# Performance work log

Hardware: AMD Instinct MI355X
Metric: run time of the kernel (lower is better)

Reference implementation:

```python
import jax, jax.numpy as jnp
import numpy as np

PSZ = 3      # patch_size
TOPK = 2     # topk candidates
EPS = 1e-12  # F.normalize eps


def extract_patches(x, psz, stride):
    """Torch unfold-style patch extraction: (B,C,H,W) -> (B, nH*nW, C, psz, psz)."""
    B, C, H, W = x.shape
    nH = (H - psz) // stride + 1
    nW = (W - psz) // stride + 1
    slices = []
    for di in range(psz):          # fixed 3x3 loop, not a data-dim loop
        for dj in range(psz):
            slices.append(x[:, :, di:di + (nH - 1) * stride + 1:stride,
                                  dj:dj + (nW - 1) * stride + 1:stride])
    p = jnp.stack(slices, axis=-1)                      # (B,C,nH,nW,psz*psz)
    p = p.reshape(B, C, nH, nW, psz, psz)
    p = p.transpose(0, 2, 3, 1, 4, 5).reshape(B, nH * nW, C, psz, psz)
    return p


def l2_normalize(x, axis):
    n = jnp.sqrt(jnp.sum(x * x, axis=axis, keepdims=True))
    return x / jnp.maximum(n, EPS)


def setup_inputs() -> dict:
    key = jax.random.key(0)
    k1, k2 = jax.random.split(key)
    pred_style = jax.random.normal(k1, (2, 128, 48, 48), dtype=jnp.float32)
    target_style = jax.random.normal(k2, (2 * TOPK, 128, 48, 48), dtype=jnp.float32)
    return {"pred_style": pred_style, "target_style": target_style}


def reference(pred_style, target_style):
    B = pred_style.shape[0]
    # raw patches (used for the final MSE / gather)
    tp = extract_patches(target_style, PSZ, 1)   # (B*TOPK, nT, C, 3, 3)
    pp = extract_patches(pred_style, PSZ, 1)     # (B, nQ, C, 3, 3)
    nT = tp.shape[1]

    # matching is done on channel-normalized features (F.normalize dim=1 / dim=2)
    p1n = extract_patches(l2_normalize(pred_style, axis=1), PSZ, 1)  # (B,nQ,C,3,3)
    tpn = l2_normalize(tp, axis=2).reshape(B, TOPK, nT, *tp.shape[2:])

    # cosine cross-correlation == conv with candidate patches as filters
    scores = jnp.einsum('bqcij,bkncij->bknq', p1n, tpn)  # (B,TOPK,nT,nQ)->(B,TOPK,nQ) reduce below

    sv = jnp.max(scores, axis=2)      # (B, TOPK, nQ) best value per candidate set
    si = jnp.argmax(scores, axis=2)   # (B, TOPK, nQ) best spatial idx per k
    k_idx = jnp.argmax(sv, axis=1)    # (B, nQ) best k per query position
    spatial = jnp.take_along_axis(si, k_idx[:, None, :], axis=1)[:, 0]  # (B, nQ)

    tpr = tp.reshape(B, TOPK, nT, *tp.shape[2:])
    bi = jnp.arange(B)[:, None]
    gathered = tpr[bi, k_idx, spatial]  # (B, nQ, C, 3, 3)

    return jnp.mean((pp - gathered) ** 2)
```

## Files before the change

### kernel.cpp

```cpp
#include <hip/hip_runtime.h>
#include <hip/hip_bf16.h>

typedef unsigned short u16;
typedef __attribute__((ext_vector_type(8))) short short8;
typedef _Float16 half8 __attribute__((ext_vector_type(8)));
typedef __attribute__((ext_vector_type(4))) float f32x4;
typedef __attribute__((ext_vector_type(4))) unsigned int u32x4;

#define CC    128
#define WW    48
#define HW2   2304
#define NHW   46
#define NQ    2116
#define NPIX  2304
#define DSTRIDE ((size_t)NPIX * NPIX + 64)
#define BATCH 2
#define MT    126
#define NTC   190
#define DTS   200

__device__ __forceinline__ u16 f2bf(float f) {
  union { float f; unsigned u; } x; x.f = f;
  unsigned r = (x.u + 0x7fffu + ((x.u >> 16) & 1u)) >> 16;
  return (u16)r;
}

__global__ __launch_bounds__(256) void k_norm(const float* __restrict__ pred,
                                              const float* __restrict__ targ,
                                              u16* __restrict__ PnT, u16* __restrict__ TnT) {
  const int img = blockIdx.y;
  const int p0  = blockIdx.x * 64;
  const int tid = threadIdx.x;
  const float* src = img < 2 ? pred + (size_t)img * CC * HW2
                             : targ + (size_t)(img - 2) * CC * HW2;
  u16* out = img < 2 ? PnT + (size_t)img * NPIX * CC
                     : TnT + (size_t)(img - 2) * NPIX * CC;

  __shared__ float sT[64][129];
  __shared__ float sInv[64];

  #pragma unroll
  for (int it = 0; it < 32; ++it) {
    int idx = it * 256 + tid;
    int c = idx >> 6, p = idx & 63;
    sT[p][c] = src[(size_t)c * HW2 + p0 + p];
  }
  __syncthreads();
  if (tid < 64) {
    float s = 0.f;
    for (int c = 0; c < CC; ++c) { float v = sT[tid][c]; s += v * v; }
    sInv[tid] = 1.0f / fmaxf(sqrtf(s), 1e-12f);
  }
  __syncthreads();
  #pragma unroll
  for (int it = 0; it < 4; ++it) {
    int cid = it * 256 + tid;
    int p = cid >> 4, g = cid & 15;
    int r = p0 + p;
    int sc = (g & ~7) | ((g & 7) ^ (r & 7));
    float inv = sInv[p];
    unsigned pack[4];
    #pragma unroll
    for (int e = 0; e < 8; ++e) {
      float v = sT[p][sc * 8 + e] * inv;
      if ((e & 1) == 0) pack[e >> 1] = (unsigned)f2bf(v);
      else              pack[e >> 1] |= ((unsigned)f2bf(v)) << 16;
    }
    u32x4 o; o.x = pack[0]; o.y = pack[1]; o.z = pack[2]; o.w = pack[3];
    *reinterpret_cast<u32x4*>(out + (size_t)r * CC + g * 8) = o;
  }
}

__global__ __launch_bounds__(512, 2) void k_pixdotH(const u16* __restrict__ PnT, const u16* __restrict__ TnT,
                                                    u16* __restrict__ H) {
  __shared__ u16 buf[40960];
  u16* sA = buf;
  u16* sB = buf + 16384;
  const int nt = blockIdx.x, mt = blockIdx.y, s = blockIdx.z;
  const int tid = threadIdx.x, lane = tid & 63, wid = tid >> 6;
  const int wm = wid >> 2, wn = wid & 3;
  const int r15 = lane & 15, g16 = lane >> 4;
  const int m0 = mt * MT, n0 = nt * NTC;

  const u16* Ab = PnT + (size_t)(s >> 1) * NPIX * CC;
  const u16* Bb = TnT + (size_t)s * NPIX * CC;
  u16* Hs = H + (size_t)s * DSTRIDE;

  #pragma unroll
  for (int i = 0; i < 4; ++i) {
    int sl = i * 512 + tid;
    int row = m0 + (sl >> 4); row = row < 2303 ? row : 2303;
    __builtin_amdgcn_global_load_lds(
      (const __attribute__((address_space(1))) unsigned*)(Ab + (size_t)row * CC + (sl & 15) * 8),
      (__attribute__((address_space(3))) unsigned*)&sA[sl * 8], 16, 0, 0);
  }
  #pragma unroll
  for (int i = 0; i < 6; ++i) {
    int sl = i * 512 + tid;
    int row = n0 + (sl >> 4); row = row < 2303 ? row : 2303;
    __builtin_amdgcn_global_load_lds(
      (const __attribute__((address_space(1))) unsigned*)(Bb + (size_t)row * CC + (sl & 15) * 8),
      (__attribute__((address_space(3))) unsigned*)&sB[sl * 8], 16, 0, 0);
  }

  f32x4 acc[4][3];
  const f32x4 z4 = {0.f, 0.f, 0.f, 0.f};
  #pragma unroll
  for (int i = 0; i < 4; ++i)
    #pragma unroll
    for (int j = 0; j < 3; ++j) acc[i][j] = z4;

  asm volatile("s_waitcnt vmcnt(0)" ::: "memory");
  __builtin_amdgcn_s_barrier();

  const int arow0 = wm * 64 + r15;
  const int brow0 = wn * 48 + r15;
  #pragma unroll
  for (int ks = 0; ks < 4; ++ks) {
    const int c = ks * 4 + g16;
    short8 af[4], bfv[3];
    #pragma unroll
    for (int mi = 0; mi < 4; ++mi) {
      int row = arow0 + mi * 16;
      int gr = m0 + row;
      af[mi] = *reinterpret_cast<const short8*>(
        &sA[row * 128 + (c >> 3) * 64 + (((c & 7) ^ (gr & 7)) * 8)]);
    }
    #pragma unroll
    for (int ni = 0; ni < 3; ++ni) {
      int row = brow0 + ni * 16;
      int gr = n0 + row;
      bfv[ni] = *reinterpret_cast<const short8*>(
        &sB[row * 128 + (c >> 3) * 64 + (((c & 7) ^ (gr & 7)) * 8)]);
    }
    __builtin_amdgcn_s_setprio(1);
    #pragma unroll
    for (int mi = 0; mi < 4; ++mi)
      #pragma unroll
      for (int ni = 0; ni < 3; ++ni)
        acc[mi][ni] = __builtin_amdgcn_mfma_f32_16x16x32_bf16(af[mi], bfv[ni], acc[mi][ni], 0, 0, 0);
    __builtin_amdgcn_s_setprio(0);
  }

  __syncthreads();
  u16* Dt = buf;
  #pragma unroll
  for (int mi = 0; mi < 4; ++mi)
    #pragma unroll
    for (int ni = 0; ni < 3; ++ni) {
      int col = wn * 48 + ni * 16 + r15;
      #pragma unroll
      for (int rg = 0; rg < 4; ++rg) {
        int row = wm * 64 + mi * 16 + g16 * 4 + rg;
        Dt[row * DTS + col] = __builtin_bit_cast(u16, (_Float16)acc[mi][ni][rg]);
      }
    }
  __syncthreads();

  for (int t = tid; t < 126 * 24; t += 512) {
    int rr = t / 24, c8 = t - rr * 24;
    int grow = m0 + rr;
    if (grow >= 2302) continue;
    int lcol = c8 * 8;
    int lim = NTC - lcol;
    int glim = 2302 - (n0 + lcol);
    lim = lim < glim ? lim : glim;
    if (lim <= 0) continue;
    int base = rr * DTS + lcol;
    half8 a0 = *reinterpret_cast<const half8*>(&Dt[base]);
    half8 b0 = *reinterpret_cast<const half8*>(&Dt[base + DTS]);
    half8 b1 = *reinterpret_cast<const half8*>(&Dt[base + DTS + 8]);
    half8 c0 = *reinterpret_cast<const half8*>(&Dt[base + 2 * DTS]);
    half8 c1 = *reinterpret_cast<const half8*>(&Dt[base + 2 * DTS + 8]);
    half8 s1v = __builtin_shufflevector(b0, b1, 1, 2, 3, 4, 5, 6, 7, 8);
    half8 s2v = __builtin_shufflevector(c0, c1, 2, 3, 4, 5, 6, 7, 8, 9);
    half8 sum = a0 + s1v + s2v;
    u32x4 pk = __builtin_bit_cast(u32x4, sum);
    u16* dst = Hs + (size_t)grow * NPIX + n0 + lcol;
    int nd = lim >= 8 ? 4 : (lim >> 1);
    #pragma unroll
    for (int d = 0; d < 4; ++d)
      if (d < nd) *reinterpret_cast<unsigned*>(dst + 2 * d) = pk[d];
  }
}

__global__ __launch_bounds__(512) void k_stencil(const u16* __restrict__ H,
                                                 const float* __restrict__ pred,
                                                 const float* __restrict__ targ,
                                                 float* __restrict__ msep) {
  const int bid = blockIdx.x;
  const int b = bid >= 1058 ? 1 : 0;
  const int j = bid - b * 1058;
  const int xcd = j & 7, pos = j >> 3;
  const int jswz = (xcd < 2 ? xcd * 133 : 266 + (xcd - 2) * 132) + pos;

  const int tid = threadIdx.x;
  const int hid = tid >> 8, htid = tid & 255;
  const int lane = tid & 63, wid = tid >> 6;
  const int q = jswz * 2 + hid;
  const int qy = q / NHW, qx = q - qy * NHW;
  const int qp = qy * WW + qx;

  const _Float16 ninf = __builtin_bit_cast(_Float16, (u16)0xFC00);
  const half8 ninf8 = {ninf, ninf, ninf, ninf, ninf, ninf, ninf, ninf};

  half8 smc[3];
  int nb[3];
  smc[0] = ninf8; smc[1] = ninf8; smc[2] = ninf8;
  nb[0] = nb[1] = nb[2] = 0;

  half8 pmax = ninf8;
  #pragma unroll
  for (int it = 0; it < 3; ++it) {
    int t = it * 256 + htid;
    if (t < 552) {
      int kc = t / 276; int rem = t - kc * 276;
      int ny = rem / 6, cx = rem - ny * 6;
      const u16* Hs = H + (size_t)(b * 2 + kc) * DSTRIDE;
      int colb = ny * 48 + cx * 8;
      half8 t0 = *reinterpret_cast<const half8*>(Hs + (size_t)qp * NPIX + colb);
      half8 t1 = *reinterpret_cast<const half8*>(Hs + (size_t)(qp + 48) * NPIX + colb + 48);
      half8 t2 = *reinterpret_cast<const half8*>(Hs + (size_t)(qp + 96) * NPIX + colb + 96);
      half8 sm = t0 + t1 + t2;
      if (cx == 5) { sm[6] = ninf; sm[7] = ninf; }
      smc[it] = sm;
      nb[it] = kc * NQ + ny * NHW + cx * 8;
      pmax = __builtin_elementwise_max(pmax, sm);
    }
  }
  float m = (float)pmax[0];
  #pragma unroll
  for (int e = 1; e < 8; ++e) { float v = (float)pmax[e]; m = v > m ? v : m; }
  #pragma unroll
  for (int off = 1; off < 64; off <<= 1) {
    float o = __shfl_xor(m, off, 64);
    m = o > m ? o : m;
  }
  __shared__ float sv[8];
  __shared__ int si[8];
  __shared__ float rsum[8];
  if (lane == 0) sv[wid] = m;
  __syncthreads();
  float M = sv[hid * 4];
  #pragma unroll
  for (int wv = 1; wv < 4; ++wv) { float v = sv[hid * 4 + wv]; M = v > M ? v : M; }

  int nmin = 0x7fffffff;
  if (m == M) {
    #pragma unroll
    for (int it = 0; it < 3; ++it) {
      #pragma unroll
      for (int e = 0; e < 8; ++e) {
        float sc = (float)smc[it][e];
        int n = nb[it] + e;
        if (sc == M && n < nmin) nmin = n;
      }
    }
  }
  #pragma unroll
  for (int off = 1; off < 64; off <<= 1) {
    int o = __shfl_xor(nmin, off, 64);
    nmin = o < nmin ? o : nmin;
  }
  if (lane == 0) si[wid] = nmin;
  __syncthreads();
  int fi = si[hid * 4];
  #pragma unroll
  for (int wv = 1; wv < 4; ++wv) { int v = si[hid * 4 + wv]; fi = v < fi ? v : fi; }

  int nkc = fi >= NQ ? 1 : 0;
  int ns = fi - nkc * NQ;
  ns = ns < NQ ? ns : NQ - 1;
  int ny = ns / NHW, nx = ns - ny * NHW;
  const float* P = pred + (size_t)b * CC * HW2;
  const float* T = targ + (size_t)(b * 2 + nkc) * CC * HW2;
  float ssum = 0.f;
  for (int i = htid; i < CC * 9; i += 256) {
    int c = i / 9, sp = i - 9 * c;
    int di = sp / 3, dj = sp - 3 * di;
    float d = P[(size_t)c * HW2 + (qy + di) * WW + qx + dj]
            - T[(size_t)c * HW2 + (ny + di) * WW + nx + dj];
    ssum += d * d;
  }
  #pragma unroll
  for (int off = 1; off < 64; off <<= 1) ssum += __shfl_xor(ssum, off, 64);
  if (lane == 0) rsum[wid] = ssum;
  __syncthreads();
  if (htid == 0) {
    float t = 0.f;
    #pragma unroll
    for (int wv = 0; wv < 4; ++wv) t += rsum[hid * 4 + wv];
    msep[b * NQ + q] = t;
  }
}

__global__ void k_final(const float* __restrict__ msep, float* __restrict__ out) {
  int t = threadIdx.x;
  float s = 0.f;
  for (int i = t; i < BATCH * NQ; i += 256) s += msep[i];
  __shared__ float red[256];
  red[t] = s; __syncthreads();
  for (int st = 128; st > 0; st >>= 1) { if (t < st) red[t] += red[t + st]; __syncthreads(); }
  if (t == 0) out[0] = red[0] * (1.0f / 4875264.0f);
}

extern "C" void kernel_launch(void* const* d_in, const int* in_sizes, int n_in,
                              void* d_out, int out_size, void* d_ws, size_t ws_size,
                              hipStream_t stream) {
  const float* pred = (const float*)d_in[0];
  const float* targ = (const float*)d_in[1];
  char* ws = (char*)d_ws;

  size_t offP = 0;
  size_t offT = offP + (size_t)2 * NPIX * CC * 2;
  size_t offH = offT + (size_t)4 * NPIX * CC * 2;
  size_t offM = offH + (size_t)4 * DSTRIDE * 2;

  u16*   PnT  = (u16*)(ws + offP);
  u16*   TnT  = (u16*)(ws + offT);
  u16*   Hbuf = (u16*)(ws + offH);
  float* msep = (float*)(ws + offM);

  k_norm<<<dim3(36, 6), 256, 0, stream>>>(pred, targ, PnT, TnT);
  k_pixdotH<<<dim3(13, 19, 4), 512, 0, stream>>>(PnT, TnT, Hbuf);
  k_stencil<<<dim3(2 * 1058), 512, 0, stream>>>(Hbuf, pred, targ, msep);
  k_final<<<1, 256, 0, stream>>>(msep, (float*)d_out);
}
```

Measured before the change: 67.39 us.

## Split K-dimension staging into halves to overlap loads with MFMA

The A and B tiles are loaded into LDS as two K-halves (channels 0-63 and 64-127) in separate buffers. The MFMAs on the first half run while the second half's global-to-LDS loads are still in flight, hiding part of the load latency. The epilogue also skips writing H rows whose pixel column is 46 or 47, which are not valid patch positions. This relies on downstream kernels never reading those rows, and it adds one extra barrier.

```diff
diff --git a/kernel.cpp b/kernel.cpp
--- a/kernel.cpp
+++ b/kernel.cpp
@@ -74,8 +74,8 @@
 __global__ __launch_bounds__(512, 2) void k_pixdotH(const u16* __restrict__ PnT, const u16* __restrict__ TnT,
                                                     u16* __restrict__ H) {
   __shared__ u16 buf[40960];
-  u16* sA = buf;
-  u16* sB = buf + 16384;
+  u16* sAh[2] = { buf, buf + 8192 };
+  u16* sBh[2] = { buf + 16384, buf + 28672 };
   const int nt = blockIdx.x, mt = blockIdx.y, s = blockIdx.z;
   const int tid = threadIdx.x, lane = tid & 63, wid = tid >> 6;
   const int wm = wid >> 2, wn = wid & 3;
@@ -86,22 +86,28 @@
   const u16* Bb = TnT + (size_t)s * NPIX * CC;
   u16* Hs = H + (size_t)s * DSTRIDE;
 
-  #pragma unroll
-  for (int i = 0; i < 4; ++i) {
-    int sl = i * 512 + tid;
-    int row = m0 + (sl >> 4); row = row < 2303 ? row : 2303;
-    __builtin_amdgcn_global_load_lds(
-      (const __attribute__((address_space(1))) unsigned*)(Ab + (size_t)row * CC + (sl & 15) * 8),
-      (__attribute__((address_space(3))) unsigned*)&sA[sl * 8], 16, 0, 0);
-  }
-  #pragma unroll
-  for (int i = 0; i < 6; ++i) {
-    int sl = i * 512 + tid;
-    int row = n0 + (sl >> 4); row = row < 2303 ? row : 2303;
-    __builtin_amdgcn_global_load_lds(
-      (const __attribute__((address_space(1))) unsigned*)(Bb + (size_t)row * CC + (sl & 15) * 8),
-      (__attribute__((address_space(3))) unsigned*)&sB[sl * 8], 16, 0, 0);
-  }
+  auto stageA = [&](int h) {
+    #pragma unroll
+    for (int i = 0; i < 2; ++i) {
+      int idx = i * 512 + tid;
+      int row = idx >> 3, lc = idx & 7;
+      int grow = m0 + row; grow = grow < 2303 ? grow : 2303;
+      __builtin_amdgcn_global_load_lds(
+        (const __attribute__((address_space(1))) unsigned*)(Ab + (size_t)grow * CC + (h * 8 + lc) * 8),
+        (__attribute__((address_space(3))) unsigned*)&sAh[h][idx * 8], 16, 0, 0);
+    }
+  };
+  auto stageB = [&](int h) {
+    #pragma unroll
+    for (int i = 0; i < 3; ++i) {
+      int idx = i * 512 + tid;
+      int row = idx >> 3, lc = idx & 7;
+      int grow = n0 + row; grow = grow < 2303 ? grow : 2303;
+      __builtin_amdgcn_global_load_lds(
+        (const __attribute__((address_space(1))) unsigned*)(Bb + (size_t)grow * CC + (h * 8 + lc) * 8),
+        (__attribute__((address_space(3))) unsigned*)&sBh[h][idx * 8], 16, 0, 0);
+    }
+  };
 
   f32x4 acc[4][3];
   const f32x4 z4 = {0.f, 0.f, 0.f, 0.f};
@@ -110,37 +116,47 @@
     #pragma unroll
     for (int j = 0; j < 3; ++j) acc[i][j] = z4;
 
+  const int arow0 = wm * 64 + r15;
+  const int brow0 = wn * 48 + r15;
+
+  auto mfmaPair = [&](int ks0) {
+    #pragma unroll
+    for (int ks = ks0; ks < ks0 + 2; ++ks) {
+      const int c = ks * 4 + g16;
+      const int h = c >> 3, lc = c & 7;
+      short8 af[4], bfv[3];
+      #pragma unroll
+      for (int mi = 0; mi < 4; ++mi) {
+        int row = arow0 + mi * 16;
+        int gr = m0 + row;
+        af[mi] = *reinterpret_cast<const short8*>(
+          &sAh[h][row * 64 + ((lc ^ (gr & 7)) * 8)]);
+      }
+      #pragma unroll
+      for (int ni = 0; ni < 3; ++ni) {
+        int row = brow0 + ni * 16;
+        int gr = n0 + row;
+        bfv[ni] = *reinterpret_cast<const short8*>(
+          &sBh[h][row * 64 + ((lc ^ (gr & 7)) * 8)]);
+      }
+      __builtin_amdgcn_s_setprio(1);
+      #pragma unroll
+      for (int mi = 0; mi < 4; ++mi)
+        #pragma unroll
+        for (int ni = 0; ni < 3; ++ni)
+          acc[mi][ni] = __builtin_amdgcn_mfma_f32_16x16x32_bf16(af[mi], bfv[ni], acc[mi][ni], 0, 0, 0);
+      __builtin_amdgcn_s_setprio(0);
+    }
+  };
+
+  stageA(0); stageB(0);
   asm volatile("s_waitcnt vmcnt(0)" ::: "memory");
   __builtin_amdgcn_s_barrier();
-
-  const int arow0 = wm * 64 + r15;
-  const int brow0 = wn * 48 + r15;
-  #pragma unroll
-  for (int ks = 0; ks < 4; ++ks) {
-    const int c = ks * 4 + g16;
-    short8 af[4], bfv[3];
-    #pragma unroll
-    for (int mi = 0; mi < 4; ++mi) {
-      int row = arow0 + mi * 16;
-      int gr = m0 + row;
-      af[mi] = *reinterpret_cast<const short8*>(
-        &sA[row * 128 + (c >> 3) * 64 + (((c & 7) ^ (gr & 7)) * 8)]);
-    }
-    #pragma unroll
-    for (int ni = 0; ni < 3; ++ni) {
-      int row = brow0 + ni * 16;
-      int gr = n0 + row;
-      bfv[ni] = *reinterpret_cast<const short8*>(
-        &sB[row * 128 + (c >> 3) * 64 + (((c & 7) ^ (gr & 7)) * 8)]);
-    }
-    __builtin_amdgcn_s_setprio(1);
-    #pragma unroll
-    for (int mi = 0; mi < 4; ++mi)
-      #pragma unroll
-      for (int ni = 0; ni < 3; ++ni)
-        acc[mi][ni] = __builtin_amdgcn_mfma_f32_16x16x32_bf16(af[mi], bfv[ni], acc[mi][ni], 0, 0, 0);
-    __builtin_amdgcn_s_setprio(0);
-  }
+  stageA(1); stageB(1);
+  mfmaPair(0);
+  asm volatile("s_waitcnt vmcnt(0)" ::: "memory");
+  __builtin_amdgcn_s_barrier();
+  mfmaPair(2);
 
   __syncthreads();
   u16* Dt = buf;
@@ -161,6 +177,7 @@
     int rr = t / 24, c8 = t - rr * 24;
     int grow = m0 + rr;
     if (grow >= 2302) continue;
+    if ((grow % 48) >= 46) continue;
     int lcol = c8 * 8;
     int lim = NTC - lcol;
     int glim = 2302 - (n0 + lcol);
```

Result: faster. 65.70 us (-2.5%).
